# Performance work log

Hardware: AMD Instinct MI355X
Metric: run time of the kernel (lower is better)

## Reference

```python
import jax, jax.numpy as jnp
import numpy as np

N_NODES = 100000
N_EDGES = 1600000
D_IN = 128
D_OUT = 128
N_RATES = 5


def setup_inputs() -> dict:
    key = jax.random.key(0)
    k1, k2, k3, k4, k5 = jax.random.split(key, 5)
    h = jax.random.normal(k1, (N_NODES, D_IN), dtype=jnp.float32)
    W = jax.random.normal(k2, (N_RATES, D_IN, D_OUT), dtype=jnp.float32) / np.sqrt(D_IN)
    b = jnp.zeros((N_RATES, D_OUT), dtype=jnp.float32)
    src = jax.random.randint(k3, (N_EDGES,), 0, N_NODES, dtype=jnp.int64)
    dst = jax.random.randint(k4, (N_EDGES,), 0, N_NODES, dtype=jnp.int64)
    rate = jax.random.randint(k5, (N_EDGES,), 0, N_RATES, dtype=jnp.int64)
    return {"h": h, "W": W, "b": b, "src": src, "dst": dst, "rate": rate}


def reference(h, W, b, src, dst, rate):
    # Per-rate edge-masked GraphConv (dgl GraphConv, norm='both'), outputs concatenated.
    # Edge subgraph is expressed as a 0/1 edge weight so shapes stay static under jit.
    N = h.shape[0]
    outs = []
    for r in range(W.shape[0]):  # small fixed set of relation types
        w_e = (rate == r).astype(h.dtype)                      # [E] subgraph mask
        out_deg = jax.ops.segment_sum(w_e, src, num_segments=N)
        in_deg = jax.ops.segment_sum(w_e, dst, num_segments=N)
        norm_src = jnp.maximum(out_deg, 1.0) ** -0.5           # dgl clamps deg to >=1
        norm_dst = jnp.maximum(in_deg, 1.0) ** -0.5
        feat = h * norm_src[:, None]                           # D_out^{-1/2} h
        msg = feat[src] * w_e[:, None]                         # gather + mask [E, D]
        agg = jax.ops.segment_sum(msg, dst, num_segments=N)    # SpMM aggregation
        outs.append((agg @ W[r]) * norm_dst[:, None] + b[r])   # weight, D_in^{-1/2}, bias
    return jnp.concatenate(outs, axis=1)                       # [N, N_RATES*D_OUT]
```

## Files before the change

### kernel.cpp

```cpp
#include <hip/hip_runtime.h>
#include <hip/hip_bf16.h>

#define N_NODES 100000
#define N_EDGES 1600000
#define DIM 128
#define N_RATES 5
#define OUT_W (N_RATES * DIM)
#define PK_SHIFT 17
#define PK_MASK  0x1FFFF
#define SCAN_NB ((N_NODES + 1023) / 1024)
#define MT_TILES ((N_NODES + 63) / 64)

#define WS_DEG_OUT 0x000000u
#define WS_DEG_IN  0x200000u
#define WS_NSRC    0x400000u
#define WS_NDST    0x600000u
#define WS_OFFS    0x800000u
#define WS_CURSOR  0x880000u
#define WS_BSUM    0x900000u
#define WS_PACKED  0xA00000u
#define WS_G       0x1100000u
#define SLOT_BYTES ((size_t)N_NODES * 256 * sizeof(unsigned short))

typedef float f4     __attribute__((ext_vector_type(4)));
typedef short bf16x8 __attribute__((ext_vector_type(8)));

__global__ __launch_bounds__(256) void deg_kernel(const int* __restrict__ src,
                                                  const int* __restrict__ dst,
                                                  const int* __restrict__ rate,
                                                  int* __restrict__ deg_out,
                                                  int* __restrict__ deg_in) {
    int e = blockIdx.x * 256 + threadIdx.x;
    if (e >= N_EDGES) return;
    int r = rate[e];
    atomicAdd(&deg_out[r * N_NODES + src[e]], 1);
    atomicAdd(&deg_in [r * N_NODES + dst[e]], 1);
}

__global__ __launch_bounds__(256) void norm_kernel(const int* __restrict__ deg_out,
                                                   const int* __restrict__ deg_in,
                                                   float* __restrict__ nsrc,
                                                   float* __restrict__ ndst) {
    int i = blockIdx.x * 256 + threadIdx.x;
    if (i >= N_RATES * N_NODES) return;
    int d0 = deg_out[i]; if (d0 < 1) d0 = 1;
    int d1 = deg_in[i];  if (d1 < 1) d1 = 1;
    nsrc[i] = 1.0f / sqrtf((float)d0);
    ndst[i] = 1.0f / sqrtf((float)d1);
}

__global__ __launch_bounds__(256) void scan1_kernel(const int* __restrict__ deg_in,
                                                    int* __restrict__ offs,
                                                    int* __restrict__ bsum) {
    __shared__ int sh[256];
    int tid = threadIdx.x;
    int base = blockIdx.x * 1024 + tid * 4;
    int v[4];
#pragma unroll
    for (int j = 0; j < 4; ++j) {
        int idx = base + j, s = 0;
        if (idx < N_NODES) {
#pragma unroll
            for (int r = 0; r < N_RATES; ++r) s += deg_in[r * N_NODES + idx];
        }
        v[j] = s;
    }
    int tsum = v[0] + v[1] + v[2] + v[3];
    sh[tid] = tsum;
    __syncthreads();
    for (int off = 1; off < 256; off <<= 1) {
        int t = (tid >= off) ? sh[tid - off] : 0;
        __syncthreads();
        sh[tid] += t;
        __syncthreads();
    }
    int excl = sh[tid] - tsum;
#pragma unroll
    for (int j = 0; j < 4; ++j) {
        int idx = base + j;
        if (idx < N_NODES) offs[idx] = excl;
        excl += v[j];
    }
    if (tid == 255) bsum[blockIdx.x] = sh[255];
}

__global__ void scan2_kernel(int* __restrict__ bsum) {
    if (threadIdx.x != 0 || blockIdx.x != 0) return;
    int run = 0;
    for (int i = 0; i < SCAN_NB; ++i) { int t = bsum[i]; bsum[i] = run; run += t; }
}

__global__ __launch_bounds__(256) void scan3_kernel(int* __restrict__ offs,
                                                    const int* __restrict__ bsum,
                                                    int* __restrict__ cursor) {
    int i = blockIdx.x * 256 + threadIdx.x;
    if (i >= N_NODES) return;
    int v = offs[i] + bsum[i >> 10];
    offs[i] = v;
    cursor[i] = v;
}

__global__ __launch_bounds__(256) void fill_kernel(const int* __restrict__ src,
                                                   const int* __restrict__ dst,
                                                   const int* __restrict__ rate,
                                                   int* __restrict__ cursor,
                                                   int* __restrict__ packed) {
    int e = blockIdx.x * 256 + threadIdx.x;
    if (e >= N_EDGES) return;
    int pos = atomicAdd(&cursor[dst[e]], 1);
    packed[pos] = src[e] | (rate[e] << PK_SHIFT);
}

template<int GS, bool ALL>
__global__ __launch_bounds__(256) void gather_kernel(const float* __restrict__ h,
                                                     const int* __restrict__ packed,
                                                     const int* __restrict__ offs,
                                                     const float* __restrict__ nsrc,
                                                     unsigned short* __restrict__ agg,
                                                     int rbase) {
    int gw   = (blockIdx.x * 256 + threadIdx.x) >> 6;
    int lane = threadIdx.x & 63;
    if (gw >= N_NODES) return;
    const int d = gw;
    int beg = offs[d];
    int end = (d == N_NODES - 1) ? N_EDGES : offs[d + 1];

    float2 a0 = make_float2(0.f, 0.f), a1 = a0, a2 = a0, a3 = a0, a4 = a0;

    int p = beg;
    for (; p + 4 <= end; p += 4) {
        int pk[4]; int rl[4]; bool use[4]; float2 v[4]; float ns[4];
#pragma unroll
        for (int i = 0; i < 4; ++i) pk[i] = packed[p + i];
#pragma unroll
        for (int i = 0; i < 4; ++i) {
            rl[i]  = (pk[i] >> PK_SHIFT) - rbase;
            use[i] = ALL || ((unsigned)rl[i] < (unsigned)GS);
        }
#pragma unroll
        for (int i = 0; i < 4; ++i) {
            int s = pk[i] & PK_MASK;
            if (use[i]) {
                v[i]  = *(const float2*)(h + (size_t)s * DIM + lane * 2);
                ns[i] = nsrc[(size_t)(rl[i] + rbase) * N_NODES + s];
            }
        }
#pragma unroll
        for (int i = 0; i < 4; ++i) {
            if (!use[i]) continue;
            float tx = v[i].x * ns[i], ty = v[i].y * ns[i];
            switch (rl[i]) {
                case 0: a0.x += tx; a0.y += ty; break;
                case 1: if constexpr (GS > 1) { a1.x += tx; a1.y += ty; } break;
                case 2: if constexpr (GS > 2) { a2.x += tx; a2.y += ty; } break;
                case 3: if constexpr (GS > 3) { a3.x += tx; a3.y += ty; } break;
                default: if constexpr (GS > 4) { a4.x += tx; a4.y += ty; } break;
            }
        }
    }
    for (; p < end; ++p) {
        int pkx = packed[p];
        int rlx = (pkx >> PK_SHIFT) - rbase;
        if (!ALL && (unsigned)rlx >= (unsigned)GS) continue;
        int s = pkx & PK_MASK;
        float2 v = *(const float2*)(h + (size_t)s * DIM + lane * 2);
        float ns = nsrc[(size_t)(rlx + rbase) * N_NODES + s];
        float tx = v.x * ns, ty = v.y * ns;
        switch (rlx) {
            case 0: a0.x += tx; a0.y += ty; break;
            case 1: if constexpr (GS > 1) { a1.x += tx; a1.y += ty; } break;
            case 2: if constexpr (GS > 2) { a2.x += tx; a2.y += ty; } break;
            case 3: if constexpr (GS > 3) { a3.x += tx; a3.y += ty; } break;
            default: if constexpr (GS > 4) { a4.x += tx; a4.y += ty; } break;
        }
    }

#pragma unroll
    for (int ri = 0; ri < GS; ++ri) {
        float2 acc = (ri == 0) ? a0 : (ri == 1) ? a1 : (ri == 2) ? a2
                   : (ri == 3) ? a3 : a4;
        unsigned short* row = agg + ((size_t)ri * N_NODES + d) * 256;
        __bf16 hx = (__bf16)acc.x; __bf16 lx = (__bf16)(acc.x - (float)hx);
        __bf16 hy = (__bf16)acc.y; __bf16 ly = (__bf16)(acc.y - (float)hy);
        unsigned int hv = (unsigned int)__builtin_bit_cast(unsigned short, hx)
                        | ((unsigned int)__builtin_bit_cast(unsigned short, hy) << 16);
        unsigned int lv = (unsigned int)__builtin_bit_cast(unsigned short, lx)
                        | ((unsigned int)__builtin_bit_cast(unsigned short, ly) << 16);
        *(unsigned int*)(row + lane * 2)       = hv;
        *(unsigned int*)(row + 128 + lane * 2) = lv;
    }
}

__global__ __launch_bounds__(256) void gemm_agg_kernel(const unsigned short* __restrict__ agg,
                                                       const float* __restrict__ Wall,
                                                       const float* __restrict__ bias,
                                                       const float* __restrict__ ndst,
                                                       float* __restrict__ out,
                                                       int rbase) {
    __shared__ __align__(16) unsigned short sWt[2][128][136];
    const int slot = blockIdx.y;
    const int r = rbase + slot;
    const float* Wr = Wall + (size_t)r * DIM * DIM;
    const int tid = threadIdx.x;

#pragma unroll
    for (int phase = 0; phase < 16; ++phase) {
        int f = phase * 1024 + tid * 4;
        int k = f >> 7, n = f & 127;
        float4 w4 = *(const float4*)(Wr + f);
        float wv[4] = {w4.x, w4.y, w4.z, w4.w};
#pragma unroll
        for (int j = 0; j < 4; ++j) {
            __bf16 hb = (__bf16)wv[j];
            __bf16 lb = (__bf16)(wv[j] - (float)hb);
            sWt[0][n + j][k] = __builtin_bit_cast(unsigned short, hb);
            sWt[1][n + j][k] = __builtin_bit_cast(unsigned short, lb);
        }
    }
    __syncthreads();

    const int w = tid >> 6, l = tid & 63;
    const int lrow = l & 15;
    const int lk   = (l >> 4) * 8;
    const int lq4  = (l >> 4) * 4;
    const float* ndr = ndst + (size_t)r * N_NODES;
    const float* br  = bias + (size_t)r * DIM;

    for (int mt = blockIdx.x; mt < MT_TILES; mt += gridDim.x) {
        int rowA = mt * 64 + w * 16 + lrow;
        int rowAc = rowA < N_NODES ? rowA : 0;
        const unsigned short* arow = agg + ((size_t)slot * N_NODES + rowAc) * 256;

        f4 acc[8];
#pragma unroll
        for (int i = 0; i < 8; ++i) acc[i] = (f4){0.f, 0.f, 0.f, 0.f};

#pragma unroll
        for (int ks = 0; ks < 4; ++ks) {
            int k0 = ks * 32;
            bf16x8 ah = *(const bf16x8*)(arow + k0 + lk);
            bf16x8 al = *(const bf16x8*)(arow + 128 + k0 + lk);
#pragma unroll
            for (int nt = 0; nt < 8; ++nt) {
                bf16x8 bh = *(const bf16x8*)&sWt[0][nt * 16 + lrow][k0 + lk];
                bf16x8 bl = *(const bf16x8*)&sWt[1][nt * 16 + lrow][k0 + lk];
                acc[nt] = __builtin_amdgcn_mfma_f32_16x16x32_bf16(ah, bh, acc[nt], 0, 0, 0);
                acc[nt] = __builtin_amdgcn_mfma_f32_16x16x32_bf16(ah, bl, acc[nt], 0, 0, 0);
                acc[nt] = __builtin_amdgcn_mfma_f32_16x16x32_bf16(al, bh, acc[nt], 0, 0, 0);
            }
        }

        int rowD0 = mt * 64 + w * 16 + lq4;
#pragma unroll
        for (int q = 0; q < 4; ++q) {
            int row = rowD0 + q;
            if (row < N_NODES) {
                float ndv = ndr[row];
                float* orow = out + (size_t)row * OUT_W + r * DIM;
#pragma unroll
                for (int nt = 0; nt < 8; ++nt) {
                    int col = nt * 16 + lrow;
                    orow[col] = acc[nt][q] * ndv + br[col];
                }
            }
        }
    }
}

__global__ __launch_bounds__(256) void zero_out_kernel(float4* __restrict__ out) {
    int i = blockIdx.x * 256 + threadIdx.x;
    if (i < N_NODES * OUT_W / 4) out[i] = make_float4(0.f, 0.f, 0.f, 0.f);
}

__global__ __launch_bounds__(256) void scatter_c_kernel(const float* __restrict__ h,
                                                        const int* __restrict__ src,
                                                        const int* __restrict__ dst,
                                                        const int* __restrict__ rate,
                                                        const float* __restrict__ nsrc,
                                                        float* __restrict__ out) {
    int lane = threadIdx.x & 63;
    int gw = (blockIdx.x * 256 + threadIdx.x) >> 6;
    int e0 = gw * 4;
#pragma unroll
    for (int i = 0; i < 4; ++i) {
        int e = e0 + i;
        if (e >= N_EDGES) return;
        int s = src[e], d = dst[e], r = rate[e];
        float ns = nsrc[(size_t)r * N_NODES + s];
        float2 v = *(const float2*)(h + (size_t)s * DIM + lane * 2);
        float* o = out + (size_t)d * OUT_W + r * DIM + lane * 2;
        unsafeAtomicAdd(o,     v.x * ns);
        unsafeAtomicAdd(o + 1, v.y * ns);
    }
}

__global__ __launch_bounds__(256) void gemm_inplace_kernel(float* __restrict__ outp,
                                                           const float* __restrict__ Wall,
                                                           const float* __restrict__ bias,
                                                           const float* __restrict__ ndst,
                                                           int r) {
    __shared__ float sW[32][128];
    __shared__ float sA[32][64];
    float* A = outp + r * DIM;
    const float* Wr = Wall + (size_t)r * DIM * DIM;
    const float* nd = ndst + (size_t)r * N_NODES;
    const float* br = bias + (size_t)r * DIM;
    int tid  = threadIdx.x;
    int row0 = blockIdx.x * 64;
    int c2   = (tid & 63) * 2;
    int rg   = tid >> 6;
    int rb   = rg * 16;
    float acc0[16], acc1[16];
#pragma unroll
    for (int i = 0; i < 16; ++i) { acc0[i] = 0.f; acc1[i] = 0.f; }
    for (int kc = 0; kc < 128; kc += 32) {
        __syncthreads();
#pragma unroll
        for (int j = 0; j < 4; ++j) {
            int f = tid * 4 + j * 1024;
            int kl = f >> 7, c = f & 127;
            *(float4*)(&sW[kl][c]) = *(const float4*)(Wr + (kc + kl) * 128 + c);
        }
#pragma unroll
        for (int j = 0; j < 2; ++j) {
            int f = tid * 4 + j * 1024;
            int rowl = f >> 5, kl = f & 31;
            int grow = row0 + rowl;
            float4 a4 = make_float4(0.f, 0.f, 0.f, 0.f);
            if (grow < N_NODES) a4 = *(const float4*)(A + (size_t)grow * OUT_W + kc + kl);
            sA[kl + 0][rowl] = a4.x; sA[kl + 1][rowl] = a4.y;
            sA[kl + 2][rowl] = a4.z; sA[kl + 3][rowl] = a4.w;
        }
        __syncthreads();
#pragma unroll
        for (int k = 0; k < 32; ++k) {
            float2 wv = *(const float2*)(&sW[k][c2]);
#pragma unroll
            for (int i = 0; i < 4; ++i) {
                float4 a = *(const float4*)(&sA[k][rb + i * 4]);
                acc0[i*4+0] += a.x * wv.x; acc1[i*4+0] += a.x * wv.y;
                acc0[i*4+1] += a.y * wv.x; acc1[i*4+1] += a.y * wv.y;
                acc0[i*4+2] += a.z * wv.x; acc1[i*4+2] += a.z * wv.y;
                acc0[i*4+3] += a.w * wv.x; acc1[i*4+3] += a.w * wv.y;
            }
        }
    }
#pragma unroll
    for (int i = 0; i < 16; ++i) {
        int row = row0 + rb + i;
        if (row < N_NODES) {
            float ndv = nd[row];
            float2 o;
            o.x = acc0[i] * ndv + br[c2];
            o.y = acc1[i] * ndv + br[c2 + 1];
            *(float2*)(A + (size_t)row * OUT_W + c2) = o;
        }
    }
}

extern "C" void kernel_launch(void* const* d_in, const int* in_sizes, int n_in,
                              void* d_out, int out_size, void* d_ws, size_t ws_size,
                              hipStream_t stream) {
    const float* h    = (const float*)d_in[0];
    const float* W    = (const float*)d_in[1];
    const float* b    = (const float*)d_in[2];
    const int*   src  = (const int*)d_in[3];
    const int*   dst  = (const int*)d_in[4];
    const int*   rate = (const int*)d_in[5];
    float* out = (float*)d_out;

    char* ws = (char*)d_ws;
    int*   deg_out = (int*)(ws + WS_DEG_OUT);
    int*   deg_in  = (int*)(ws + WS_DEG_IN);
    float* nsrc    = (float*)(ws + WS_NSRC);
    float* ndst    = (float*)(ws + WS_NDST);
    int*   offs    = (int*)(ws + WS_OFFS);
    int*   cursor  = (int*)(ws + WS_CURSOR);
    int*   bsum    = (int*)(ws + WS_BSUM);
    int*   packed  = (int*)(ws + WS_PACKED);
    unsigned short* agg = (unsigned short*)(ws + WS_G);

    int n_slots = 0;
    if (ws_size > WS_G) n_slots = (int)((ws_size - WS_G) / SLOT_BYTES);
    if (n_slots > N_RATES) n_slots = N_RATES;

    hipMemsetAsync(ws, 0, 0x400000, stream);
    deg_kernel<<<(N_EDGES + 255) / 256, 256, 0, stream>>>(src, dst, rate, deg_out, deg_in);
    norm_kernel<<<(N_RATES * N_NODES + 255) / 256, 256, 0, stream>>>(deg_out, deg_in,
                                                                     nsrc, ndst);

    if (n_slots >= 1) {
        scan1_kernel<<<SCAN_NB, 256, 0, stream>>>(deg_in, offs, bsum);
        scan2_kernel<<<1, 1, 0, stream>>>(bsum);
        scan3_kernel<<<(N_NODES + 255) / 256, 256, 0, stream>>>(offs, bsum, cursor);
        fill_kernel<<<(N_EDGES + 255) / 256, 256, 0, stream>>>(src, dst, rate,
                                                               cursor, packed);
        const int ggrid = (N_NODES * 64 + 255) / 256;
        int done = 0;
        while (done < N_RATES) {
            int gs = N_RATES - done; if (gs > n_slots) gs = n_slots;
            switch (gs) {
                case 5: gather_kernel<5, true ><<<ggrid, 256, 0, stream>>>(h, packed, offs,
                                                                           nsrc, agg, done); break;
                case 4: gather_kernel<4, false><<<ggrid, 256, 0, stream>>>(h, packed, offs,
                                                                           nsrc, agg, done); break;
                case 3: gather_kernel<3, false><<<ggrid, 256, 0, stream>>>(h, packed, offs,
                                                                           nsrc, agg, done); break;
                case 2: gather_kernel<2, false><<<ggrid, 256, 0, stream>>>(h, packed, offs,
                                                                           nsrc, agg, done); break;
                default: gather_kernel<1, false><<<ggrid, 256, 0, stream>>>(h, packed, offs,
                                                                            nsrc, agg, done); break;
            }
            gemm_agg_kernel<<<dim3(256, gs), 256, 0, stream>>>(agg, W, b, ndst, out, done);
            done += gs;
        }
    } else {
        zero_out_kernel<<<(N_NODES * OUT_W / 4 + 255) / 256, 256, 0, stream>>>((float4*)out);
        scatter_c_kernel<<<(N_EDGES / 4 * 64 + 255) / 256, 256, 0, stream>>>(h, src, dst,
                                                                             rate, nsrc, out);
        for (int r = 0; r < N_RATES; ++r)
            gemm_inplace_kernel<<<(N_NODES + 63) / 64, 256, 0, stream>>>(out, W, b, ndst, r);
    }
}
```

Baseline: 965.3 us.

## Unroll gather by 8, double GEMM row tile, pre-swizzle W in LDS

```diff
diff --git a/kernel.cpp b/kernel.cpp
--- a/kernel.cpp
+++ b/kernel.cpp
@@ -9,7 +9,8 @@
 #define PK_SHIFT 17
 #define PK_MASK  0x1FFFF
 #define SCAN_NB ((N_NODES + 1023) / 1024)
-#define MT_TILES ((N_NODES + 63) / 64)
+#define MT2_TILES ((N_NODES + 127) / 128)
+#define GEMM_GX 391
 
 #define WS_DEG_OUT 0x000000u
 #define WS_DEG_IN  0x200000u
@@ -128,17 +129,17 @@
     float2 a0 = make_float2(0.f, 0.f), a1 = a0, a2 = a0, a3 = a0, a4 = a0;
 
     int p = beg;
-    for (; p + 4 <= end; p += 4) {
-        int pk[4]; int rl[4]; bool use[4]; float2 v[4]; float ns[4];
-#pragma unroll
-        for (int i = 0; i < 4; ++i) pk[i] = packed[p + i];
-#pragma unroll
-        for (int i = 0; i < 4; ++i) {
+    for (; p + 8 <= end; p += 8) {
+        int pk[8]; int rl[8]; bool use[8]; float2 v[8]; float ns[8];
+#pragma unroll
+        for (int i = 0; i < 8; ++i) pk[i] = packed[p + i];
+#pragma unroll
+        for (int i = 0; i < 8; ++i) {
             rl[i]  = (pk[i] >> PK_SHIFT) - rbase;
             use[i] = ALL || ((unsigned)rl[i] < (unsigned)GS);
         }
 #pragma unroll
-        for (int i = 0; i < 4; ++i) {
+        for (int i = 0; i < 8; ++i) {
             int s = pk[i] & PK_MASK;
             if (use[i]) {
                 v[i]  = *(const float2*)(h + (size_t)s * DIM + lane * 2);
@@ -146,7 +147,7 @@
             }
         }
 #pragma unroll
-        for (int i = 0; i < 4; ++i) {
+        for (int i = 0; i < 8; ++i) {
             if (!use[i]) continue;
             float tx = v[i].x * ns[i], ty = v[i].y * ns[i];
             switch (rl[i]) {
@@ -197,7 +198,7 @@
                                                        const float* __restrict__ ndst,
                                                        float* __restrict__ out,
                                                        int rbase) {
-    __shared__ __align__(16) unsigned short sWt[2][128][136];
+    __shared__ __align__(16) unsigned short sB[4][8][2][64][8];
     const int slot = blockIdx.y;
     const int r = rbase + slot;
     const float* Wr = Wall + (size_t)r * DIM * DIM;
@@ -208,13 +209,19 @@
         int f = phase * 1024 + tid * 4;
         int k = f >> 7, n = f & 127;
         float4 w4 = *(const float4*)(Wr + f);
+        int ks = k >> 5;
+        int lhi16 = ((k & 31) >> 3) * 16;
+        int j = k & 7;
         float wv[4] = {w4.x, w4.y, w4.z, w4.w};
 #pragma unroll
-        for (int j = 0; j < 4; ++j) {
-            __bf16 hb = (__bf16)wv[j];
-            __bf16 lb = (__bf16)(wv[j] - (float)hb);
-            sWt[0][n + j][k] = __builtin_bit_cast(unsigned short, hb);
-            sWt[1][n + j][k] = __builtin_bit_cast(unsigned short, lb);
+        for (int j4 = 0; j4 < 4; ++j4) {
+            int col = n + j4;
+            int nt = col >> 4;
+            int lanew = lhi16 + (col & 15);
+            __bf16 hb = (__bf16)wv[j4];
+            __bf16 lb = (__bf16)(wv[j4] - (float)hb);
+            sB[ks][nt][0][lanew][j] = __builtin_bit_cast(unsigned short, hb);
+            sB[ks][nt][1][lanew][j] = __builtin_bit_cast(unsigned short, lb);
         }
     }
     __syncthreads();
@@ -226,41 +233,53 @@
     const float* ndr = ndst + (size_t)r * N_NODES;
     const float* br  = bias + (size_t)r * DIM;
 
-    for (int mt = blockIdx.x; mt < MT_TILES; mt += gridDim.x) {
-        int rowA = mt * 64 + w * 16 + lrow;
-        int rowAc = rowA < N_NODES ? rowA : 0;
-        const unsigned short* arow = agg + ((size_t)slot * N_NODES + rowAc) * 256;
-
-        f4 acc[8];
-#pragma unroll
-        for (int i = 0; i < 8; ++i) acc[i] = (f4){0.f, 0.f, 0.f, 0.f};
+    for (int mt = blockIdx.x; mt < MT2_TILES; mt += GEMM_GX) {
+        int rowA0 = mt * 128 + w * 32 + lrow;
+        int rowA1 = rowA0 + 16;
+        int r0c = rowA0 < N_NODES ? rowA0 : 0;
+        int r1c = rowA1 < N_NODES ? rowA1 : 0;
+        const unsigned short* a0p = agg + ((size_t)slot * N_NODES + r0c) * 256;
+        const unsigned short* a1p = agg + ((size_t)slot * N_NODES + r1c) * 256;
+
+        f4 acc0[8], acc1[8];
+#pragma unroll
+        for (int i = 0; i < 8; ++i) { acc0[i] = (f4){0.f,0.f,0.f,0.f}; acc1[i] = acc0[i]; }
 
 #pragma unroll
         for (int ks = 0; ks < 4; ++ks) {
-            int k0 = ks * 32;
-            bf16x8 ah = *(const bf16x8*)(arow + k0 + lk);
-            bf16x8 al = *(const bf16x8*)(arow + 128 + k0 + lk);
+            int k0 = ks * 32 + lk;
+            bf16x8 a0h = *(const bf16x8*)(a0p + k0);
+            bf16x8 a0l = *(const bf16x8*)(a0p + 128 + k0);
+            bf16x8 a1h = *(const bf16x8*)(a1p + k0);
+            bf16x8 a1l = *(const bf16x8*)(a1p + 128 + k0);
 #pragma unroll
             for (int nt = 0; nt < 8; ++nt) {
-                bf16x8 bh = *(const bf16x8*)&sWt[0][nt * 16 + lrow][k0 + lk];
-                bf16x8 bl = *(const bf16x8*)&sWt[1][nt * 16 + lrow][k0 + lk];
-                acc[nt] = __builtin_amdgcn_mfma_f32_16x16x32_bf16(ah, bh, acc[nt], 0, 0, 0);
-                acc[nt] = __builtin_amdgcn_mfma_f32_16x16x32_bf16(ah, bl, acc[nt], 0, 0, 0);
-                acc[nt] = __builtin_amdgcn_mfma_f32_16x16x32_bf16(al, bh, acc[nt], 0, 0, 0);
-            }
-        }
-
-        int rowD0 = mt * 64 + w * 16 + lq4;
-#pragma unroll
-        for (int q = 0; q < 4; ++q) {
-            int row = rowD0 + q;
-            if (row < N_NODES) {
-                float ndv = ndr[row];
-                float* orow = out + (size_t)row * OUT_W + r * DIM;
-#pragma unroll
-                for (int nt = 0; nt < 8; ++nt) {
-                    int col = nt * 16 + lrow;
-                    orow[col] = acc[nt][q] * ndv + br[col];
+                bf16x8 bh = *(const bf16x8*)&sB[ks][nt][0][l][0];
+                bf16x8 bl = *(const bf16x8*)&sB[ks][nt][1][l][0];
+                acc0[nt] = __builtin_amdgcn_mfma_f32_16x16x32_bf16(a0h, bh, acc0[nt], 0, 0, 0);
+                acc0[nt] = __builtin_amdgcn_mfma_f32_16x16x32_bf16(a0h, bl, acc0[nt], 0, 0, 0);
+                acc0[nt] = __builtin_amdgcn_mfma_f32_16x16x32_bf16(a0l, bh, acc0[nt], 0, 0, 0);
+                acc1[nt] = __builtin_amdgcn_mfma_f32_16x16x32_bf16(a1h, bh, acc1[nt], 0, 0, 0);
+                acc1[nt] = __builtin_amdgcn_mfma_f32_16x16x32_bf16(a1h, bl, acc1[nt], 0, 0, 0);
+                acc1[nt] = __builtin_amdgcn_mfma_f32_16x16x32_bf16(a1l, bh, acc1[nt], 0, 0, 0);
+            }
+        }
+
+        int rowD0 = mt * 128 + w * 32 + lq4;
+#pragma unroll
+        for (int half = 0; half < 2; ++half) {
+#pragma unroll
+            for (int q = 0; q < 4; ++q) {
+                int row = rowD0 + half * 16 + q;
+                if (row < N_NODES) {
+                    float ndv = ndr[row];
+                    float* orow = out + (size_t)row * OUT_W + r * DIM;
+#pragma unroll
+                    for (int nt = 0; nt < 8; ++nt) {
+                        int col = nt * 16 + lrow;
+                        f4 a = half ? acc1[nt] : acc0[nt];
+                        orow[col] = a[q] * ndv + br[col];
+                    }
                 }
             }
         }
@@ -411,7 +430,7 @@
                 default: gather_kernel<1, false><<<ggrid, 256, 0, stream>>>(h, packed, offs,
                                                                             nsrc, agg, done); break;
             }
-            gemm_agg_kernel<<<dim3(256, gs), 256, 0, stream>>>(agg, W, b, ndst, out, done);
+            gemm_agg_kernel<<<dim3(GEMM_GX, gs), 256, 0, stream>>>(agg, W, b, ndst, out, done);
             done += gs;
         }
     } else {
```

Result: no change. 952.4 us (-1.3%).
